# Optimization experiments

Hardware: AMD Instinct MI355X
Metric: run time of the kernel (lower is better)

Reference implementation:

```python
import jax, jax.numpy as jnp
import numpy as np

ALPHA = 0.2        # APPNP teleport
LEAKY = 0.2        # leaky_relu slope in GAT
NEG_INF = -1.0e9   # additive mask value


def setup_inputs() -> dict:
    key = jax.random.key(0)
    ks = jax.random.split(key, 6)
    B, N, I, H, O = 108, 392, 256, 4, 64
    x = jax.random.normal(ks[0], (B, N, I), dtype=jnp.float32)
    # fully-connected GCN-preprocessed adjacency: D^-1/2 (A) D^-1/2 of ones == 1/N
    a = jnp.ones((N, N), dtype=jnp.float32) / N
    w_mlp = jax.random.normal(ks[1], (I, I), dtype=jnp.float32) * (1.0 / np.sqrt(I))
    b_mlp = jnp.zeros((I,), dtype=jnp.float32)
    kernel = jax.random.normal(ks[2], (I, H, O), dtype=jnp.float32) * (1.0 / np.sqrt(I))
    attn_self_k = jax.random.normal(ks[3], (O, H, 1), dtype=jnp.float32) * 0.1
    attn_neigh_k = jax.random.normal(ks[4], (O, H, 1), dtype=jnp.float32) * 0.1
    bias = jnp.zeros((H * O,), dtype=jnp.float32)
    return {"x": x, "a": a, "w_mlp": w_mlp, "b_mlp": b_mlp, "kernel": kernel,
            "attn_self_k": attn_self_k, "attn_neigh_k": attn_neigh_k, "bias": bias}


def _gnn_core(x, a, w_mlp, b_mlp, kernel, attn_self_k, attn_neigh_k, bias):
    # ---- APPNPConv (1 propagation, sigmoid MLP) ----
    mlp_out = jax.nn.sigmoid(jnp.einsum('bni,io->bno', x, w_mlp) + b_mlp)
    z = (1.0 - ALPHA) * jnp.einsum('nm,bmf->bnf', a, mlp_out) + ALPHA * mlp_out
    # ---- GATConvPatched._call_dense ----
    n = a.shape[-1]
    eye = jnp.eye(n, dtype=a.dtype)
    a_sl = jnp.where(eye > 0, jnp.ones((), a.dtype), a)   # set_diag(a, 1) = add self loops
    xp = jnp.einsum('bni,iho->bnho', z, kernel)           # [B,N,H,O]
    s = jnp.einsum('bnho,oht->bnht', xp, attn_self_k)     # [B,N,H,1]
    ng = jnp.einsum('bnho,oht->bnht', xp, attn_neigh_k)   # [B,N,H,1]
    ng_t = jnp.transpose(ng, (0, 3, 2, 1))                # '...ABC->...CBA' -> [B,1,H,N]
    coef = jax.nn.leaky_relu(s + ng_t, negative_slope=LEAKY)   # [B,N,H,N]
    mask_logits = jnp.where(a_sl == 0.0, NEG_INF, 0.0)    # [N,N]
    coef = coef + mask_logits[:, None, :]                 # broadcast over batch & heads
    attn = jax.nn.softmax(coef, axis=-1)
    # dropout is identity at inference
    out = jnp.einsum('bnhm,bmhi->bnhi', attn, xp)         # [B,N,H,O]
    B, N_, H, O = out.shape
    out = out.reshape(B, N_, H * O) + bias                # concat heads + bias
    return jax.nn.elu(out)                                # gat_activation='elu'


def reference(x, a, w_mlp, b_mlp, kernel, attn_self_k, attn_neigh_k, bias):
    return _gnn_core(x, a, w_mlp, b_mlp, kernel, attn_self_k, attn_neigh_k, bias)
```

## Files before the change

### kernel.cpp

```cpp
#include <hip/hip_runtime.h>
#include <hip/hip_bf16.h>
#include <math.h>
#include <float.h>

#define BATCH 108
#define NNODE 392
#define IDIM  256
#define HEADS 4
#define ODIM  64
#define HO    256
#define MROWS (BATCH*NNODE)
#define SGH   (BATCH*HEADS*NNODE)

typedef __attribute__((ext_vector_type(8))) short bf16x8;
typedef __attribute__((ext_vector_type(8))) unsigned short u16x8;
typedef __attribute__((ext_vector_type(4))) float f32x4;

__device__ __forceinline__ ushort f2bf(float f) {
    unsigned u = __float_as_uint(f);
    unsigned r = (u + 0x7FFFu + ((u >> 16) & 1u)) >> 16;
    return (ushort)r;
}
__device__ __forceinline__ float bf2f(ushort h) {
    return __uint_as_float(((unsigned)h) << 16);
}
__device__ __forceinline__ float fsigmoid(float x) {
    float e = __expf(-x);
    return __builtin_amdgcn_rcpf(1.0f + e);
}

#define MSTR 264

#define FRAG(src, jn, k0t) \
    (*(const bf16x8*)((src) + ((((wg * 4 + (jn)) * 8 + (k0t)) << 9)) + lane * 8))

__global__ __launch_bounds__(256)
void fused_gemm(const float* __restrict__ x, const ushort* __restrict__ wshuf,
                const ushort* __restrict__ kshuf, const float* __restrict__ bmlp,
                float* __restrict__ zbacc, ushort* __restrict__ xp0,
                const float* __restrict__ askv, const float* __restrict__ ankv,
                float* __restrict__ s0, float* __restrict__ ng0)
{
    __shared__ __attribute__((aligned(16))) ushort AsMs[32 * MSTR];
    __shared__ float cs_lds[256];

    const int t    = threadIdx.x;
    const int lane = t & 63;
    const int wg   = t >> 6;
    const int lr   = lane & 15, kq = lane >> 4;
    const int rb   = blockIdx.x;
    const int b    = blockIdx.y;
    const int row0 = rb * 32;
    const long gbase = (long)b * NNODE;

    bf16x8 wreg[2][4];
    #pragma unroll
    for (int jn = 0; jn < 4; ++jn) {
        wreg[0][jn] = FRAG(wshuf, jn, 0);
        wreg[1][jn] = FRAG(wshuf, jn, 1);
    }

    {
        const float* xb = x + (gbase + row0) * 256;
        #pragma unroll
        for (int j = 0; j < 8; ++j) {
            int e4  = t + j * 256;
            int row = e4 >> 6;
            int col = (e4 & 63) * 4;
            float4 v = (row0 + row < NNODE)
                ? *(const float4*)(xb + (long)row * 256 + col)
                : make_float4(0.f, 0.f, 0.f, 0.f);
            *(ushort4*)&AsMs[row * MSTR + col] =
                make_ushort4(f2bf(v.x), f2bf(v.y), f2bf(v.z), f2bf(v.w));
        }
    }
    __syncthreads();

    f32x4 acc[4][2] = {};

    {
        #pragma unroll
        for (int k0t = 0; k0t < 8; ++k0t) {
            bf16x8 xf0 = *(const bf16x8*)&AsMs[lr * MSTR + k0t * 32 + kq * 8];
            bf16x8 xf1 = *(const bf16x8*)&AsMs[(16 + lr) * MSTR + k0t * 32 + kq * 8];
            #pragma unroll
            for (int jn = 0; jn < 4; ++jn) {
                acc[jn][0] = __builtin_amdgcn_mfma_f32_16x16x32_bf16(
                    wreg[k0t & 1][jn], xf0, acc[jn][0], 0, 0, 0);
                acc[jn][1] = __builtin_amdgcn_mfma_f32_16x16x32_bf16(
                    wreg[k0t & 1][jn], xf1, acc[jn][1], 0, 0, 0);
            }
            if (k0t < 6) {
                #pragma unroll
                for (int jn = 0; jn < 4; ++jn)
                    wreg[k0t & 1][jn] = FRAG(wshuf, jn, k0t + 2);
            }
        }
    }

    bf16x8 kreg[2][4];
    #pragma unroll
    for (int jn = 0; jn < 4; ++jn) kreg[0][jn] = FRAG(kshuf, jn, 0);

    __syncthreads();

    {
        float4 bi[4];
        #pragma unroll
        for (int jn = 0; jn < 4; ++jn)
            bi[jn] = *(const float4*)(bmlp + 64 * wg + 16 * jn + 4 * kq);
        float cs[4][4] = {};
        #pragma unroll
        for (int imL = 0; imL < 2; ++imL) {
            const int r_ = 16 * imL + lr;
            const bool ok = row0 + r_ < NNODE;
            #pragma unroll
            for (int jn = 0; jn < 4; ++jn) {
                float v[4];
                v[0] = fsigmoid(acc[jn][imL][0] + bi[jn].x);
                v[1] = fsigmoid(acc[jn][imL][1] + bi[jn].y);
                v[2] = fsigmoid(acc[jn][imL][2] + bi[jn].z);
                v[3] = fsigmoid(acc[jn][imL][3] + bi[jn].w);
                *(ushort4*)&AsMs[r_ * MSTR + 64 * wg + 16 * jn + 4 * kq] =
                    make_ushort4(f2bf(v[0]), f2bf(v[1]), f2bf(v[2]), f2bf(v[3]));
                if (ok) {
                    cs[jn][0] += v[0]; cs[jn][1] += v[1];
                    cs[jn][2] += v[2]; cs[jn][3] += v[3];
                }
            }
        }
        #pragma unroll
        for (int jn = 0; jn < 4; ++jn)
            #pragma unroll
            for (int r = 0; r < 4; ++r) {
                float v = cs[jn][r];
                v += __shfl_xor(v, 1, 64);
                v += __shfl_xor(v, 2, 64);
                v += __shfl_xor(v, 4, 64);
                v += __shfl_xor(v, 8, 64);
                if (lr == 0)
                    cs_lds[64 * wg + 16 * jn + 4 * kq + r] = v;
            }
    }
    __syncthreads();

    #pragma unroll
    for (int jn = 0; jn < 4; ++jn)
        #pragma unroll
        for (int imL = 0; imL < 2; ++imL)
            acc[jn][imL] = f32x4{0.f, 0.f, 0.f, 0.f};

    #pragma unroll
    for (int jn = 0; jn < 4; ++jn) kreg[1][jn] = FRAG(kshuf, jn, 1);

    {
        #pragma unroll
        for (int k0t = 0; k0t < 8; ++k0t) {
            bf16x8 xf0 = *(const bf16x8*)&AsMs[lr * MSTR + k0t * 32 + kq * 8];
            bf16x8 xf1 = *(const bf16x8*)&AsMs[(16 + lr) * MSTR + k0t * 32 + kq * 8];
            #pragma unroll
            for (int jn = 0; jn < 4; ++jn) {
                acc[jn][0] = __builtin_amdgcn_mfma_f32_16x16x32_bf16(
                    kreg[k0t & 1][jn], xf0, acc[jn][0], 0, 0, 0);
                acc[jn][1] = __builtin_amdgcn_mfma_f32_16x16x32_bf16(
                    kreg[k0t & 1][jn], xf1, acc[jn][1], 0, 0, 0);
            }
            if (k0t < 6) {
                #pragma unroll
                for (int jn = 0; jn < 4; ++jn)
                    kreg[k0t & 1][jn] = FRAG(kshuf, jn, k0t + 2);
            }
        }
    }

    {
        const int h = wg;
        float askr[4][4], ankr[4][4];
        #pragma unroll
        for (int jn = 0; jn < 4; ++jn)
            #pragma unroll
            for (int r = 0; r < 4; ++r) {
                int o = 16 * jn + 4 * kq + r;
                askr[jn][r] = askv[o * HEADS + h];
                ankr[jn][r] = ankv[o * HEADS + h];
            }
        #pragma unroll
        for (int imL = 0; imL < 2; ++imL) {
            const int r_ = 16 * imL + lr;
            const int lrow = row0 + r_;
            const bool ok = lrow < NNODE;
            float ps = 0.0f, pn = 0.0f;
            if (ok) {
                ushort* dst = xp0 + (gbase + lrow) * 256 + 64 * h + 4 * kq;
                #pragma unroll
                for (int jn = 0; jn < 4; ++jn) {
                    float v0 = 0.2f * acc[jn][imL][0];
                    float v1 = 0.2f * acc[jn][imL][1];
                    float v2 = 0.2f * acc[jn][imL][2];
                    float v3 = 0.2f * acc[jn][imL][3];
                    *(ushort4*)(dst + 16 * jn) =
                        make_ushort4(f2bf(v0), f2bf(v1), f2bf(v2), f2bf(v3));
                    ps += v0 * askr[jn][0] + v1 * askr[jn][1] +
                          v2 * askr[jn][2] + v3 * askr[jn][3];
                    pn += v0 * ankr[jn][0] + v1 * ankr[jn][1] +
                          v2 * ankr[jn][2] + v3 * ankr[jn][3];
                }
            }
            ps += __shfl_xor(ps, 16, 64);
            ps += __shfl_xor(ps, 32, 64);
            pn += __shfl_xor(pn, 16, 64);
            pn += __shfl_xor(pn, 32, 64);
            if (ok && kq == 0) {
                long si = ((long)b * HEADS + h) * NNODE + lrow;
                s0[si]  = ps;
                ng0[si] = pn;
            }
        }
    }

    atomicAdd(&zbacc[b * 256 + t], cs_lds[t]);
}

__global__ __launch_bounds__(256)
void wcvt(const float* __restrict__ w_mlp, const float* __restrict__ kern,
          ushort* __restrict__ wshuf, ushort* __restrict__ kshuf,
          float* __restrict__ zbacc)
{
    if (blockIdx.x < BATCH)
        zbacc[blockIdx.x * 256 + threadIdx.x] = 0.0f;
    long idx = (long)(blockIdx.x & 255) * 256 + threadIdx.x;
    const float* src = (blockIdx.x < 256) ? w_mlp : kern;
    ushort* dst = (blockIdx.x < 256) ? wshuf : kshuf;
    int e    = idx & 7;
    int lane = (int)(idx >> 3) & 63;
    int k0t  = (int)(idx >> 9) & 7;
    int jn   = (int)(idx >> 12) & 3;
    int g    = (int)(idx >> 14);
    int n = 64 * g + 16 * jn + (lane & 15);
    int k = 32 * k0t + (lane >> 4) * 8 + e;
    dst[idx] = f2bf(src[(long)k * 256 + n]);
}

__global__ __launch_bounds__(512)
void attn_stats(const float* __restrict__ s0, const float* __restrict__ ng0,
                const float* __restrict__ zbacc, const float* __restrict__ kern,
                const float* __restrict__ askv, const float* __restrict__ ankv,
                uint* __restrict__ ptG, float2* __restrict__ w12G,
                float2* __restrict__ g12G)
{
    __shared__ float key[512];
    __shared__ int   perm[512];
    __shared__ float w1[NNODE], w2[NNODE];
    __shared__ float D1[NNODE + 1], D2[NNODE + 1];
    __shared__ float zsh[IDIM];
    __shared__ float partK[8][64];
    __shared__ float wsumA[8], wsumB[8];
    __shared__ float scs[2];

    const int t = threadIdx.x;
    const int bh = blockIdx.x;
    const int b = bh >> 2, h = bh & 3;
    const long base = (long)bh * NNODE;
    const int ln = t & 63, w = t >> 6;

    if (t < IDIM) zsh[t] = zbacc[b * 256 + t] * (0.8f / (float)NNODE);
    __syncthreads();
    {
        const int o = ln, kc = w;
        float p = 0.0f;
        #pragma unroll
        for (int kk = 0; kk < 32; ++kk) {
            int k = kc * 32 + kk;
            p = fmaf(zsh[k], kern[(long)k * HO + h * 64 + o], p);
        }
        partK[kc][o] = p;
    }
    __syncthreads();
    if (t < 64) {
        float zk = 0.0f;
        #pragma unroll
        for (int kc = 0; kc < 8; ++kc) zk += partK[kc][t];
        float ps = zk * askv[t * HEADS + h];
        float pn = zk * ankv[t * HEADS + h];
        #pragma unroll
        for (int off = 32; off; off >>= 1) {
            ps += __shfl_down(ps, off, 64);
            pn += __shfl_down(pn, off, 64);
        }
        if (t == 0) { scs[0] = ps; scs[1] = pn; }
    }
    __syncthreads();
    const float sc = scs[0], ngc = scs[1];

    float rk = (t < NNODE) ? (ng0[base + t] + ngc) : FLT_MAX;
    int   rp = t;

    for (int k = 2; k <= 512; k <<= 1) {
        for (int j = k >> 1; j > 0; j >>= 1) {
            const bool dir = ((t & k) == 0);
            const bool lower = ((t & j) == 0);
            float ok_; int op;
            if (j >= 64) {
                __syncthreads();
                key[t] = rk; perm[t] = rp;
                __syncthreads();
                ok_ = key[t ^ j];
                op  = perm[t ^ j];
            } else {
                ok_ = __shfl_xor(rk, j, 64);
                op  = __shfl_xor(rp, j, 64);
            }
            const bool sw = lower ? ((rk > ok_) == dir) : ((ok_ > rk) == dir);
            if (sw) { rk = ok_; rp = op; }
        }
    }
    __syncthreads();
    key[t] = rk; perm[t] = rp;

    const float w1v = (t < NNODE) ? __expf(rk) : 0.0f;
    const float w2v = (t < NNODE) ? __expf(0.2f * rk) : 0.0f;
    if (t < NNODE) { w1[t] = w1v; w2[t] = w2v; }

    float v1 = w1v;
    #pragma unroll
    for (int s = 1; s < 64; s <<= 1) {
        float tmp = __shfl_down(v1, s, 64);
        if (ln + s < 64) v1 += tmp;
    }
    float v2 = (ln >= 1) ? __shfl_up(w2v, 1, 64) : 0.0f;
    #pragma unroll
    for (int s = 1; s < 64; s <<= 1) {
        float tmp = __shfl_up(v2, s, 64);
        if (ln >= s) v2 += tmp;
    }
    const float wt2 = __shfl(v2, 63, 64) + __shfl(w2v, 63, 64);
    if (ln == 0) { wsumA[w] = v1; wsumB[w] = wt2; }
    __syncthreads();
    {
        float off1 = 0.0f, off2 = 0.0f;
        for (int ww = w + 1; ww < 8; ++ww) off1 += wsumA[ww];
        for (int ww = 0; ww < w; ++ww)     off2 += wsumB[ww];
        if (t < NNODE) {
            D1[t] = v1 + off1;
            D2[t] = v2 + off2;
        }
        if (t == 0) {
            D1[NNODE] = 0.0f;
            float tot = 0.0f;
            #pragma unroll
            for (int ww = 0; ww < 8; ++ww) tot += wsumB[ww];
            D2[NNODE] = tot;
        }
    }
    __syncthreads();

    if (t < NNODE) {
        float sn = s0[base + t] + sc;
        float negs = -sn;
        int lo = 0, hi = NNODE;
        while (lo < hi) {
            int mid = (lo + hi) >> 1;
            if (key[mid] < negs) lo = mid + 1; else hi = mid;
        }
        float e1 = __expf(sn), e2 = __expf(0.2f * sn);
        float inv = __builtin_amdgcn_rcpf(e1 * D1[lo] + e2 * D2[lo]);
        ptG[base + t]  = (uint)perm[t] | ((uint)lo << 16);
        g12G[base + t] = make_float2(e1 * inv, e2 * inv);
        w12G[base + t] = make_float2(w1[t], w2[t]);
    }
}

#define CHN 7
#define NP  (NNODE + 1)
__global__ __launch_bounds__(1024)
void attn_scan(const ushort* __restrict__ xp, const uint* __restrict__ ptG,
               const float2* __restrict__ w12G, const float2* __restrict__ g12G,
               const float* __restrict__ zbacc, const float* __restrict__ kern,
               const float* __restrict__ bias, float* __restrict__ out)
{
    __shared__ float  Vs[16 * NP];
    __shared__ float  S1[16 * NP];
    __shared__ float  w1s[NNODE], w2s[NNODE], g1s[NNODE], g2s[NNODE];
    __shared__ ushort perms[NNODE], tls[NNODE];
    __shared__ float  CT[64][17], CT2[64][17];
    __shared__ float  zsh[IDIM];
    __shared__ float  bp[16][17];
    __shared__ float  biasl[16];

    const int t  = threadIdx.x;
    const int og = blockIdx.x;
    const int bh = blockIdx.y;
    const int b  = bh >> 2, h = bh & 3;
    const long base = (long)bh * NNODE;
    const int c0 = h * 64 + og * 16;

    if (t < NNODE) {
        uint pt = ptG[base + t];
        perms[t] = (ushort)(pt & 0xFFFFu);
        tls[t]   = (ushort)(pt >> 16);
        float2 w = w12G[base + t];
        w1s[t] = w.x; w2s[t] = w.y;
    } else if (t >= 512 && t < 512 + NNODE) {
        int i = t - 512;
        float2 g = g12G[base + i];
        g1s[i] = g.x; g2s[i] = g.y;
    }
    if (t < IDIM) zsh[t] = zbacc[b * 256 + t] * (0.8f / (float)NNODE);
    __syncthreads();

    if (t < 256) {
        const int o2 = t & 15, g = t >> 4;
        float p = 0.0f;
        #pragma unroll
        for (int kk = 0; kk < 16; ++kk) {
            int k = 16 * g + kk;
            p = fmaf(zsh[k], kern[(long)k * HO + c0 + o2], p);
        }
        bp[g][o2] = p;
    }

    if (t < NNODE * 2) {
        int j = t >> 1, q = (t & 1) * 8;
        int m = perms[j];
        u16x8 raw = *(const u16x8*)(xp + ((long)b * NNODE + m) * HO + c0 + q);
        #pragma unroll
        for (int oo = 0; oo < 8; ++oo) Vs[(q + oo) * NP + j] = bf2f(raw[oo]);
    }
    __syncthreads();

    if (t < 16) {
        float s = bias[c0 + t];
        #pragma unroll
        for (int g = 0; g < 16; ++g) s += bp[g][t];
        biasl[t] = s;
    }

    const int c = t >> 4, o = t & 15;

    {
        float acc = 0.0f;
        #pragma unroll
        for (int jj = CHN - 1; jj >= 0; --jj) {
            int j = c * CHN + jj;
            if (j < NNODE) {
                acc = fmaf(w1s[j], Vs[o * NP + j], acc);
                S1[o * NP + j] = acc;
            }
        }
        CT[c][o] = acc;
    }
    __syncthreads();
    {
        const int w = t >> 6, ln = t & 63;
        float v = CT[ln][w];
        #pragma unroll
        for (int s = 1; s < 64; s <<= 1) {
            float tmp = __shfl_down(v, s, 64);
            if (ln + s < 64) v += tmp;
        }
        CT[ln][w] = v;
    }
    __syncthreads();
    {
        float off = (c < 63) ? CT[c + 1][o] : 0.0f;
        #pragma unroll
        for (int jj = 0; jj < CHN; ++jj) {
            int j = c * CHN + jj;
            if (j < NNODE) S1[o * NP + j] += off;
        }
        if (c == 0) S1[o * NP + NNODE] = 0.0f;
    }
    {
        float acc = 0.0f;
        #pragma unroll
        for (int jj = 0; jj < CHN; ++jj) {
            int j = c * CHN + jj;
            if (j < NNODE) {
                float tmp = Vs[o * NP + j];
                Vs[o * NP + j] = acc;
                acc = fmaf(w2s[j], tmp, acc);
            }
        }
        CT2[c][o] = acc;
    }
    __syncthreads();
    {
        const int w = t >> 6, ln = t & 63;
        float v = CT2[ln][w];
        #pragma unroll
        for (int s = 1; s < 64; s <<= 1) {
            float tmp = __shfl_up(v, s, 64);
            if (ln >= s) v += tmp;
        }
        CT2[ln][w] = v;
    }
    __syncthreads();
    {
        float off = (c > 0) ? CT2[c - 1][o] : 0.0f;
        #pragma unroll
        for (int jj = 0; jj < CHN; ++jj) {
            int j = c * CHN + jj;
            if (j < NNODE) Vs[o * NP + j] += off;
        }
        if (c == 63) Vs[o * NP + NNODE] = CT2[63][o];
    }
    __syncthreads();

    for (int idx = t; idx < NNODE * 4; idx += 1024) {
        int n = idx >> 2, q = (idx & 3) * 4;
        int tt = tls[n];
        float g1 = g1s[n], g2 = g2s[n];
        float r[4];
        #pragma unroll
        for (int rr = 0; rr < 4; ++rr) {
            int oo = q + rr;
            float v = g1 * S1[oo * NP + tt] + g2 * Vs[oo * NP + tt] + biasl[oo];
            r[rr] = (v > 0.0f) ? v : (__expf(v) - 1.0f);
        }
        *(float4*)(out + ((long)b * NNODE + n) * HO + c0 + q) =
            make_float4(r[0], r[1], r[2], r[3]);
    }
}

extern "C" void kernel_launch(void* const* d_in, const int* in_sizes, int n_in,
                              void* d_out, int out_size, void* d_ws, size_t ws_size,
                              hipStream_t stream) {
    const float* x     = (const float*)d_in[0];
    const float* w_mlp = (const float*)d_in[2];
    const float* b_mlp = (const float*)d_in[3];
    const float* kern  = (const float*)d_in[4];
    const float* ask   = (const float*)d_in[5];
    const float* ank   = (const float*)d_in[6];
    const float* bias  = (const float*)d_in[7];
    float* out = (float*)d_out;

    const long TENS = (long)MROWS * IDIM;
    float*  s0    = (float*)d_ws;
    float*  ng0   = s0 + SGH;
    float*  zbacc = ng0 + SGH;
    float2* w12G  = (float2*)(zbacc + (long)BATCH * IDIM);
    float2* g12G  = w12G + SGH;
    uint*   ptG   = (uint*)(g12G + SGH);
    ushort* xp_bf = (ushort*)(ptG + SGH);
    ushort* wshuf = xp_bf + TENS;
    ushort* kshuf = wshuf + 65536;

    dim3 blk(256);

    wcvt<<<dim3(512), blk, 0, stream>>>(w_mlp, kern, wshuf, kshuf, zbacc);

    fused_gemm<<<dim3(13, BATCH), dim3(256), 0, stream>>>(
        x, wshuf, kshuf, b_mlp, zbacc, xp_bf, ask, ank, s0, ng0);

    attn_stats<<<dim3(BATCH * HEADS), dim3(512), 0, stream>>>(
        s0, ng0, zbacc, kern, ask, ank, ptG, w12G, g12G);

    attn_scan<<<dim3(4, BATCH * HEADS), dim3(1024), 0, stream>>>(
        xp_bf, ptG, w12G, g12G, zbacc, kern, bias, out);
}
```

Before: 177.4 us.

## Fuse attention stats and scan kernels into one per-(batch,head) kernel

Merges attn_stats and attn_scan into a single kernel that keeps the sort permutation, softmax weights and gate factors in shared memory. The block then loops over the head's 64 output columns in 8-column chunks to do the prefix scans and write the output. This removes the global round trip for ptG/w12G/g12G, one kernel launch, and the per-column-group recomputation of the bias projection. In exchange it uses 432 blocks of 512 threads instead of 1728 blocks of 1024, so there is less parallelism and a longer serial loop with many barriers per block.

New measurement: 183.5 us. +3.4%, slower.

```diff
diff --git a/kernel.cpp b/kernel.cpp
--- a/kernel.cpp
+++ b/kernel.cpp
@@ -241,45 +241,52 @@
     dst[idx] = f2bf(src[(long)k * 256 + n]);
 }
 
+#define NP  (NNODE + 1)
 __global__ __launch_bounds__(512)
-void attn_stats(const float* __restrict__ s0, const float* __restrict__ ng0,
+void attn_fused(const float* __restrict__ s0, const float* __restrict__ ng0,
                 const float* __restrict__ zbacc, const float* __restrict__ kern,
                 const float* __restrict__ askv, const float* __restrict__ ankv,
-                uint* __restrict__ ptG, float2* __restrict__ w12G,
-                float2* __restrict__ g12G)
+                const ushort* __restrict__ xp, const float* __restrict__ bias,
+                float* __restrict__ out)
 {
-    __shared__ float key[512];
-    __shared__ int   perm[512];
-    __shared__ float w1[NNODE], w2[NNODE];
-    __shared__ float D1[NNODE + 1], D2[NNODE + 1];
-    __shared__ float zsh[IDIM];
-    __shared__ float partK[8][64];
-    __shared__ float wsumA[8], wsumB[8];
-    __shared__ float scs[2];
-
-    const int t = threadIdx.x;
+    __shared__ float  key[512];
+    __shared__ int    perm[512];
+    __shared__ float  w1[NNODE], w2[NNODE];
+    __shared__ float  D1[NNODE + 1], D2[NNODE + 1];
+    __shared__ float  g1s[NNODE], g2s[NNODE];
+    __shared__ ushort tls[NNODE];
+    __shared__ float  biasl[64];
+    __shared__ float  Vs[8 * NP];
+    __shared__ float  S1[8 * NP];
+    __shared__ float  CT[64][9], CT2[64][9];
+    __shared__ float  zsh[IDIM];
+    __shared__ float  partK[8][64];
+    __shared__ float  wsumA[8], wsumB[8];
+    __shared__ float  scs[2];
+
+    const int t  = threadIdx.x;
     const int bh = blockIdx.x;
-    const int b = bh >> 2, h = bh & 3;
+    const int b  = bh >> 2, h = bh & 3;
     const long base = (long)bh * NNODE;
     const int ln = t & 63, w = t >> 6;
 
     if (t < IDIM) zsh[t] = zbacc[b * 256 + t] * (0.8f / (float)NNODE);
     __syncthreads();
     {
-        const int o = ln, kc = w;
         float p = 0.0f;
         #pragma unroll
         for (int kk = 0; kk < 32; ++kk) {
-            int k = kc * 32 + kk;
-            p = fmaf(zsh[k], kern[(long)k * HO + h * 64 + o], p);
-        }
-        partK[kc][o] = p;
+            int k = w * 32 + kk;
+            p = fmaf(zsh[k], kern[(long)k * HO + h * 64 + ln], p);
+        }
+        partK[w][ln] = p;
     }
     __syncthreads();
     if (t < 64) {
         float zk = 0.0f;
         #pragma unroll
         for (int kc = 0; kc < 8; ++kc) zk += partK[kc][t];
+        biasl[t] = bias[h * 64 + t] + zk;
         float ps = zk * askv[t * HEADS + h];
         float pn = zk * ankv[t * HEADS + h];
         #pragma unroll
@@ -364,161 +371,107 @@
         }
         float e1 = __expf(sn), e2 = __expf(0.2f * sn);
         float inv = __builtin_amdgcn_rcpf(e1 * D1[lo] + e2 * D2[lo]);
-        ptG[base + t]  = (uint)perm[t] | ((uint)lo << 16);
-        g12G[base + t] = make_float2(e1 * inv, e2 * inv);
-        w12G[base + t] = make_float2(w1[t], w2[t]);
-    }
-}
-
-#define CHN 7
-#define NP  (NNODE + 1)
-__global__ __launch_bounds__(1024)
-void attn_scan(const ushort* __restrict__ xp, const uint* __restrict__ ptG,
-               const float2* __restrict__ w12G, const float2* __restrict__ g12G,
-               const float* __restrict__ zbacc, const float* __restrict__ kern,
-               const float* __restrict__ bias, float* __restrict__ out)
-{
-    __shared__ float  Vs[16 * NP];
-    __shared__ float  S1[16 * NP];
-    __shared__ float  w1s[NNODE], w2s[NNODE], g1s[NNODE], g2s[NNODE];
-    __shared__ ushort perms[NNODE], tls[NNODE];
-    __shared__ float  CT[64][17], CT2[64][17];
-    __shared__ float  zsh[IDIM];
-    __shared__ float  bp[16][17];
-    __shared__ float  biasl[16];
-
-    const int t  = threadIdx.x;
-    const int og = blockIdx.x;
-    const int bh = blockIdx.y;
-    const int b  = bh >> 2, h = bh & 3;
-    const long base = (long)bh * NNODE;
-    const int c0 = h * 64 + og * 16;
-
-    if (t < NNODE) {
-        uint pt = ptG[base + t];
-        perms[t] = (ushort)(pt & 0xFFFFu);
-        tls[t]   = (ushort)(pt >> 16);
-        float2 w = w12G[base + t];
-        w1s[t] = w.x; w2s[t] = w.y;
-    } else if (t >= 512 && t < 512 + NNODE) {
-        int i = t - 512;
-        float2 g = g12G[base + i];
-        g1s[i] = g.x; g2s[i] = g.y;
-    }
-    if (t < IDIM) zsh[t] = zbacc[b * 256 + t] * (0.8f / (float)NNODE);
-    __syncthreads();
-
-    if (t < 256) {
-        const int o2 = t & 15, g = t >> 4;
-        float p = 0.0f;
-        #pragma unroll
-        for (int kk = 0; kk < 16; ++kk) {
-            int k = 16 * g + kk;
-            p = fmaf(zsh[k], kern[(long)k * HO + c0 + o2], p);
-        }
-        bp[g][o2] = p;
-    }
-
-    if (t < NNODE * 2) {
-        int j = t >> 1, q = (t & 1) * 8;
-        int m = perms[j];
-        u16x8 raw = *(const u16x8*)(xp + ((long)b * NNODE + m) * HO + c0 + q);
-        #pragma unroll
-        for (int oo = 0; oo < 8; ++oo) Vs[(q + oo) * NP + j] = bf2f(raw[oo]);
-    }
-    __syncthreads();
-
-    if (t < 16) {
-        float s = bias[c0 + t];
-        #pragma unroll
-        for (int g = 0; g < 16; ++g) s += bp[g][t];
-        biasl[t] = s;
-    }
-
-    const int c = t >> 4, o = t & 15;
-
-    {
-        float acc = 0.0f;
-        #pragma unroll
-        for (int jj = CHN - 1; jj >= 0; --jj) {
-            int j = c * CHN + jj;
-            if (j < NNODE) {
-                acc = fmaf(w1s[j], Vs[o * NP + j], acc);
-                S1[o * NP + j] = acc;
-            }
-        }
-        CT[c][o] = acc;
-    }
-    __syncthreads();
-    {
-        const int w = t >> 6, ln = t & 63;
-        float v = CT[ln][w];
-        #pragma unroll
-        for (int s = 1; s < 64; s <<= 1) {
-            float tmp = __shfl_down(v, s, 64);
-            if (ln + s < 64) v += tmp;
-        }
-        CT[ln][w] = v;
-    }
-    __syncthreads();
-    {
-        float off = (c < 63) ? CT[c + 1][o] : 0.0f;
-        #pragma unroll
-        for (int jj = 0; jj < CHN; ++jj) {
-            int j = c * CHN + jj;
-            if (j < NNODE) S1[o * NP + j] += off;
-        }
-        if (c == 0) S1[o * NP + NNODE] = 0.0f;
-    }
-    {
-        float acc = 0.0f;
-        #pragma unroll
-        for (int jj = 0; jj < CHN; ++jj) {
-            int j = c * CHN + jj;
-            if (j < NNODE) {
-                float tmp = Vs[o * NP + j];
-                Vs[o * NP + j] = acc;
-                acc = fmaf(w2s[j], tmp, acc);
-            }
-        }
-        CT2[c][o] = acc;
-    }
-    __syncthreads();
-    {
-        const int w = t >> 6, ln = t & 63;
-        float v = CT2[ln][w];
-        #pragma unroll
-        for (int s = 1; s < 64; s <<= 1) {
-            float tmp = __shfl_up(v, s, 64);
-            if (ln >= s) v += tmp;
-        }
-        CT2[ln][w] = v;
-    }
-    __syncthreads();
-    {
-        float off = (c > 0) ? CT2[c - 1][o] : 0.0f;
-        #pragma unroll
-        for (int jj = 0; jj < CHN; ++jj) {
-            int j = c * CHN + jj;
-            if (j < NNODE) Vs[o * NP + j] += off;
-        }
-        if (c == 63) Vs[o * NP + NNODE] = CT2[63][o];
-    }
-    __syncthreads();
-
-    for (int idx = t; idx < NNODE * 4; idx += 1024) {
-        int n = idx >> 2, q = (idx & 3) * 4;
-        int tt = tls[n];
-        float g1 = g1s[n], g2 = g2s[n];
-        float r[4];
-        #pragma unroll
-        for (int rr = 0; rr < 4; ++rr) {
-            int oo = q + rr;
-            float v = g1 * S1[oo * NP + tt] + g2 * Vs[oo * NP + tt] + biasl[oo];
-            r[rr] = (v > 0.0f) ? v : (__expf(v) - 1.0f);
-        }
-        *(float4*)(out + ((long)b * NNODE + n) * HO + c0 + q) =
-            make_float4(r[0], r[1], r[2], r[3]);
+        g1s[t] = e1 * inv;
+        g2s[t] = e2 * inv;
+        tls[t] = (ushort)lo;
+    }
+    __syncthreads();
+
+    const int c = t >> 3, o = t & 7;
+    for (int og2 = 0; og2 < 8; ++og2) {
+        const int c0 = h * 64 + og2 * 8;
+
+        if (t < NNODE) {
+            int m = perm[t];
+            u16x8 raw = *(const u16x8*)(xp + ((long)b * NNODE + m) * HO + c0);
+            #pragma unroll
+            for (int oo = 0; oo < 8; ++oo) Vs[oo * NP + t] = bf2f(raw[oo]);
+        }
+        __syncthreads();
+
+        {
+            float acc = 0.0f;
+            #pragma unroll
+            for (int jj = 7 - 1; jj >= 0; --jj) {
+                int j = c * 7 + jj;
+                if (j < NNODE) {
+                    acc = fmaf(w1[j], Vs[o * NP + j], acc);
+                    S1[o * NP + j] = acc;
+                }
+            }
+            CT[c][o] = acc;
+        }
+        __syncthreads();
+        {
+            float v = CT[ln][w];
+            #pragma unroll
+            for (int s = 1; s < 64; s <<= 1) {
+                float tmp = __shfl_down(v, s, 64);
+                if (ln + s < 64) v += tmp;
+            }
+            CT[ln][w] = v;
+        }
+        __syncthreads();
+        {
+            float off = (c < 63) ? CT[c + 1][o] : 0.0f;
+            #pragma unroll
+            for (int jj = 0; jj < 7; ++jj) {
+                int j = c * 7 + jj;
+                if (j < NNODE) S1[o * NP + j] += off;
+            }
+            if (c == 0) S1[o * NP + NNODE] = 0.0f;
+        }
+        {
+            float acc = 0.0f;
+            #pragma unroll
+            for (int jj = 0; jj < 7; ++jj) {
+                int j = c * 7 + jj;
+                if (j < NNODE) {
+                    float tmp = Vs[o * NP + j];
+                    Vs[o * NP + j] = acc;
+                    acc = fmaf(w2[j], tmp, acc);
+                }
+            }
+            CT2[c][o] = acc;
+        }
+        __syncthreads();
+        {
+            float v = CT2[ln][w];
+            #pragma unroll
+            for (int s = 1; s < 64; s <<= 1) {
+                float tmp = __shfl_up(v, s, 64);
+                if (ln >= s) v += tmp;
+            }
+            CT2[ln][w] = v;
+        }
+        __syncthreads();
+        {
+            float off = (c > 0) ? CT2[c - 1][o] : 0.0f;
+            #pragma unroll
+            for (int jj = 0; jj < 7; ++jj) {
+                int j = c * 7 + jj;
+                if (j < NNODE) Vs[o * NP + j] += off;
+            }
+            if (c == 63) Vs[o * NP + NNODE] = CT2[63][o];
+        }
+        __syncthreads();
+
+        for (int idx = t; idx < NNODE * 2; idx += 512) {
+            int n = idx >> 1, q = (idx & 1) * 4;
+            int tt = tls[n];
+            float g1 = g1s[n], g2 = g2s[n];
+            float r[4];
+            #pragma unroll
+            for (int rr = 0; rr < 4; ++rr) {
+                int oo = q + rr;
+                float v = g1 * S1[oo * NP + tt] + g2 * Vs[oo * NP + tt] +
+                          biasl[og2 * 8 + oo];
+                r[rr] = (v > 0.0f) ? v : (__expf(v) - 1.0f);
+            }
+            *(float4*)(out + ((long)b * NNODE + n) * HO + c0 + q) =
+                make_float4(r[0], r[1], r[2], r[3]);
+        }
+        __syncthreads();
     }
 }
 
@@ -538,10 +491,7 @@
     float*  s0    = (float*)d_ws;
     float*  ng0   = s0 + SGH;
     float*  zbacc = ng0 + SGH;
-    float2* w12G  = (float2*)(zbacc + (long)BATCH * IDIM);
-    float2* g12G  = w12G + SGH;
-    uint*   ptG   = (uint*)(g12G + SGH);
-    ushort* xp_bf = (ushort*)(ptG + SGH);
+    ushort* xp_bf = (ushort*)(zbacc + (long)BATCH * IDIM);
     ushort* wshuf = xp_bf + TENS;
     ushort* kshuf = wshuf + 65536;
 
@@ -552,9 +502,6 @@
     fused_gemm<<<dim3(13, BATCH), dim3(256), 0, stream>>>(
         x, wshuf, kshuf, b_mlp, zbacc, xp_bf, ask, ank, s0, ng0);
 
-    attn_stats<<<dim3(BATCH * HEADS), dim3(512), 0, stream>>>(
-        s0, ng0, zbacc, kern, ask, ank, ptG, w12G, g12G);
-
-    attn_scan<<<dim3(4, BATCH * HEADS), dim3(1024), 0, stream>>>(
-        xp_bf, ptG, w12G, g12G, zbacc, kern, bias, out);
-}
+    attn_fused<<<dim3(BATCH * HEADS), dim3(512), 0, stream>>>(
+        s0, ng0, zbacc, kern, ask, ank, xp_bf, bias, out);
+}
```
